# Kernel tuning notes

Measured on AMD Instinct MI355X. Metric: run time of the kernel, lower is better.

The kernel has to match this reference:

```python
import jax, jax.numpy as jnp
import numpy as np

B, N, D, H = 8192, 9, 1024, 4096
# query_type '3p': num_layer=3, edges (h_ind, r_ind, t_ind), no negation, simple_graph=False
EDGES = [(2, 3, 4), (4, 5, 6), (6, 7, 8)]
NUM_LAYER = 3
EPS = 0.1


def setup_inputs() -> dict:
    key = jax.random.key(0)
    k1, k2, k3 = jax.random.split(key, 3)
    scale1 = 1.0 / np.sqrt(D)
    scale2 = 1.0 / np.sqrt(H)
    return {
        "node_embedding": jax.random.normal(k1, (B, N, D), dtype=jnp.float32),
        "W1": jax.random.normal(k2, (D, H), dtype=jnp.float32) * scale1,
        "b1": jnp.zeros((H,), dtype=jnp.float32),
        "W2": jax.random.normal(k3, (H, D), dtype=jnp.float32) * scale2,
        "b2": jnp.zeros((D,), dtype=jnp.float32),
    }


def reference(node_embedding, W1, b1, W2, b2):
    # message passing: for each edge, tail gets estimate_tail(h, r) = h + r,
    # head gets estimate_head(t, r) = t - r (mp_lhs=True, mp_rel=False).
    # The num_layer loop re-appends identical messages, so sum = NUM_LAYER * per-edge sum.
    msgs = {}
    for h, r, t in EDGES:
        he = node_embedding[:, h]   # [B, D]
        re_ = node_embedding[:, r]
        te = node_embedding[:, t]
        msgs.setdefault(t, []).append(he + re_)   # estimate_tail_emb
        msgs.setdefault(h, []).append(te - re_)   # estimate_head_emb

    def mlp(x):
        return jax.nn.relu(x @ W1 + b1) @ W2 + b2

    terms = sorted(msgs.keys())  # [2, 4, 6, 8] for '3p'
    outs = []
    for t in terms:
        agg = NUM_LAYER * sum(msgs[t]) + node_embedding[:, t] * EPS  # agg_func='sum'
        outs.append(mlp(agg))
    return jnp.stack(outs, axis=0)  # [num_terms, B, D]
```

## Files before the change

kernel.cpp:

```cpp
#include <hip/hip_runtime.h>
#include <hip/hip_bf16.h>

typedef __hip_bfloat16 bf16;
typedef __attribute__((ext_vector_type(8))) short short8;
typedef __attribute__((ext_vector_type(4))) short short4v;
typedef __attribute__((ext_vector_type(4))) float floatx4;

#define BQ 8192
#define ND 9
#define DD 1024
#define HH 4096
#define MM 32768

__device__ __forceinline__ short f2bf(float f) {
  unsigned u = __float_as_uint(f);
  u = (u + 0x7fff + ((u >> 16) & 1)) >> 16;
  return (short)u;
}

__device__ __forceinline__ void async16(const void* g, void* l) {
  __builtin_amdgcn_global_load_lds(
      (const __attribute__((address_space(1))) void*)g,
      (__attribute__((address_space(3))) void*)l, 16, 0, 0);
}

__global__ __launch_bounds__(256) void build_x(const float* __restrict__ emb,
                                               bf16* __restrict__ X) {
  int b = blockIdx.x;
  int d = threadIdx.x * 4;
  const float* base = emb + (size_t)b * (ND * DD) + d;

  float e[7][4];
#pragma unroll
  for (int k = 0; k < 7; ++k) *(float4*)e[k] = *(const float4*)(base + (k + 2) * DD);

  auto store = [&](int t, const float* v) {
    short4v o;
#pragma unroll
    for (int c = 0; c < 4; ++c) o[c] = f2bf(v[c]);
    *(short4v*)(X + ((size_t)t * BQ + b) * DD + d) = o;
  };

  float o0[4], o1[4], o2[4], o3[4];
#pragma unroll
  for (int c = 0; c < 4; ++c) {
    o0[c] = 0.1f * e[0][c] - 3.f * e[1][c] + 3.f * e[2][c];
    o1[c] = 3.f * e[0][c] + 3.f * e[1][c] + 0.1f * e[2][c] - 3.f * e[3][c] + 3.f * e[4][c];
    o2[c] = 3.f * e[2][c] + 3.f * e[3][c] + 0.1f * e[4][c] - 3.f * e[5][c] + 3.f * e[6][c];
    o3[c] = 3.f * e[4][c] + 3.f * e[5][c] + 0.1f * e[6][c];
  }
  store(0, o0); store(1, o1); store(2, o2); store(3, o3);
}

__global__ void transpose_f2b(const float* __restrict__ src, bf16* __restrict__ dst,
                              int rows, int cols) {
  __shared__ float t[32][33];
  int c0 = blockIdx.x * 32, r0 = blockIdx.y * 32;
  int tx = threadIdx.x, ty = threadIdx.y;
  t[ty][tx] = src[(size_t)(r0 + ty) * cols + (c0 + tx)];
  __syncthreads();
  short v = f2bf(t[tx][ty]);
  dst[(size_t)(c0 + ty) * rows + (r0 + tx)] = *(bf16*)&v;
}

template <int RELU, typename OutT, int K, int N, int LOGNX>
__global__ __launch_bounds__(512, 2) void gemm256(const bf16* __restrict__ A,
                                                  const bf16* __restrict__ Bt,
                                                  const float* __restrict__ bias,
                                                  OutT* __restrict__ C) {
  constexpr int NT = K / 64;
  __shared__ bf16 sm[65536];
  char* smc = (char*)sm;
  const bf16* smb = (const bf16*)sm;

  const int tid = threadIdx.x;
  const int l = tid & 63;
  const int wv = tid >> 6;

  const int G = gridDim.x;
  const int bid = blockIdx.x;
  const int gb = (bid & 7) * (G >> 3) + (bid >> 3);
  const int n0 = (gb & ((1 << LOGNX) - 1)) * 256;
  const int m0 = (gb >> LOGNX) * 256;

  const int rowb = wv * 8 + (l >> 3);
  const int kx = ((l & 7) ^ ((l >> 3) & 7)) << 3;
  const bf16* pA = A + (size_t)(m0 + rowb) * K + kx;
  const bf16* pB = Bt + (size_t)(n0 + rowb) * K + kx;
  const int wlo = wv * 1024;

  const int ra = ((wv >> 1) * 32 + (l & 15)) * 64;
  const int rb = ((wv & 1) * 64 + (l & 15)) * 64;
  const int kg = l >> 4;
  const int sx = l & 7;

  floatx4 acc[4][8];
#pragma unroll
  for (int q = 0; q < 4; ++q)
#pragma unroll
    for (int f = 0; f < 8; ++f)
#pragma unroll
      for (int r = 0; r < 4; ++r) acc[q][f][r] = 0.f;

#define STG(GP, LO)                                            \
  do {                                                         \
    async16((GP), smc + (LO) + wlo);                           \
    async16((GP) + (size_t)64 * K, smc + (LO) + wlo + 8192);   \
  } while (0)

#define RD_A(dst, REG, BUFE)                                                   \
  _Pragma("unroll") for (int mf = 0; mf < 2; ++mf)                             \
  _Pragma("unroll") for (int ks = 0; ks < 2; ++ks)                             \
      dst[mf][ks] = *(const short8*)(smb + (BUFE) + (REG) + ra + mf * 1024 +   \
                                     ((((ks << 2) + kg) ^ sx) << 3));

#define RD_B(dst, REG, BUFE)                                                   \
  _Pragma("unroll") for (int nf = 0; nf < 4; ++nf)                             \
  _Pragma("unroll") for (int ks = 0; ks < 2; ++ks)                             \
      dst[nf][ks] = *(const short8*)(smb + (BUFE) + (REG) + rb + nf * 1024 +   \
                                     ((((ks << 2) + kg) ^ sx) << 3));

#define MF(AF, BF, Q)                                                          \
  __builtin_amdgcn_s_setprio(1);                                               \
  _Pragma("unroll") for (int ks = 0; ks < 2; ++ks)                             \
  _Pragma("unroll") for (int mf = 0; mf < 2; ++mf)                             \
  _Pragma("unroll") for (int nf = 0; nf < 4; ++nf)                             \
      acc[Q][mf * 4 + nf] = __builtin_amdgcn_mfma_f32_16x16x32_bf16(           \
          AF[mf][ks], BF[nf][ks], acc[Q][mf * 4 + nf], 0, 0, 0);               \
  __builtin_amdgcn_s_setprio(0);

#define TILE(tt, EC, BN)                                                       \
  do {                                                                         \
    short8 a0[2][2], a1[2][2], b0[4][2], b1[4][2];                             \
    RD_A(a0, 0, EC);                                                           \
    RD_B(b0, 16384, EC);                                                       \
    RD_A(a1, 8192, EC);                                                        \
    RD_B(b1, 24576, EC);                                                       \
    if ((tt) + 1 < NT) {                                                       \
      const size_t ko = (size_t)((tt) + 1) * 64;                               \
      STG(pA + ko, BN);                                                        \
      STG(pA + (size_t)128 * K + ko, (BN) + 16384);                            \
      STG(pB + ko, (BN) + 32768);                                              \
      STG(pB + (size_t)128 * K + ko, (BN) + 49152);                            \
    }                                                                          \
    MF(a0, b0, 0);                                                             \
    MF(a1, b0, 1);                                                             \
    MF(a1, b1, 2);                                                             \
    MF(a0, b1, 3);                                                             \
    __syncthreads();                                                           \
  } while (0)

  STG(pA, 0);
  STG(pA + (size_t)128 * K, 16384);
  STG(pB, 32768);
  STG(pB + (size_t)128 * K, 49152);
  __syncthreads();

#pragma unroll 1
  for (int t = 0; t < NT; t += 2) {
    TILE(t, 0, 65536);
    TILE(t + 1, 32768, 0);
  }

  const int col0 = n0 + (wv & 1) * 64 + (l & 15);
  const int row0 = m0 + (wv >> 1) * 32 + ((l >> 4) << 2);
#pragma unroll
  for (int q = 0; q < 4; ++q) {
    const int qa = (q == 1 || q == 2) ? 1 : 0;
    const int qb = (q >= 2) ? 1 : 0;
#pragma unroll
    for (int nf = 0; nf < 4; ++nf) {
      const int col = col0 + qb * 128 + nf * 16;
      const float bv = bias[col];
#pragma unroll
      for (int mf = 0; mf < 2; ++mf) {
#pragma unroll
        for (int r = 0; r < 4; ++r) {
          const int row = row0 + qa * 128 + mf * 16 + r;
          float v = acc[q][mf * 4 + nf][r] + bv;
          if (RELU) v = fmaxf(v, 0.f);
          if constexpr (sizeof(OutT) == 2) {
            short s = f2bf(v);
            C[(size_t)row * N + col] = *(OutT*)&s;
          } else {
            C[(size_t)row * N + col] = *(OutT*)&v;
          }
        }
      }
    }
  }
#undef STG
#undef RD_A
#undef RD_B
#undef MF
#undef TILE
}

extern "C" void kernel_launch(void* const* d_in, const int* in_sizes, int n_in,
                              void* d_out, int out_size, void* d_ws, size_t ws_size,
                              hipStream_t stream) {
  const float* emb = (const float*)d_in[0];
  const float* W1  = (const float*)d_in[1];
  const float* b1  = (const float*)d_in[2];
  const float* W2  = (const float*)d_in[3];
  const float* b2  = (const float*)d_in[4];
  float* out = (float*)d_out;

  char* ws = (char*)d_ws;
  bf16* X   = (bf16*)(ws);
  bf16* Y   = (bf16*)(ws + (size_t)67108864);
  bf16* W1t = (bf16*)(ws + (size_t)67108864 + (size_t)268435456);
  bf16* W2t = (bf16*)(ws + (size_t)67108864 + (size_t)268435456 + (size_t)8388608);

  build_x<<<dim3(BQ), dim3(256), 0, stream>>>(emb, X);
  transpose_f2b<<<dim3(HH / 32, DD / 32), dim3(32, 32), 0, stream>>>(W1, W1t, DD, HH);
  transpose_f2b<<<dim3(DD / 32, HH / 32), dim3(32, 32), 0, stream>>>(W2, W2t, HH, DD);
  gemm256<1, bf16, DD, HH, 4><<<dim3((MM / 256) * (HH / 256)), dim3(512), 0, stream>>>(X, W1t, b1, Y);
  gemm256<0, float, HH, DD, 2><<<dim3((MM / 256) * (DD / 256)), dim3(512), 0, stream>>>(Y, W2t, b2, out);
}
```

Measured before the change: 1.141 ms.

## Restructure GEMM main loop into phased ping-pong schedule with finer-grained prefetch

Replaces the two-tile unrolled loop, which issued all next-tile loads and then ran a full syncthreads, with a per-iteration four-phase schedule. Each phase reads one quarter of the LDS fragments, issues one sub-tile global-to-LDS load (some two tiles ahead), then runs an MFMA block between explicit s_barriers and sched_barriers. Manual vmcnt waits let loads stay in flight across iterations. The aim is better overlap of global loads, LDS reads and MFMA work, at the cost of more barriers per tile and fragile buffer-reuse ordering.

After: 938.0 us. 1.22x faster.

```diff
diff --git a/kernel.cpp b/kernel.cpp
--- a/kernel.cpp
+++ b/kernel.cpp
@@ -108,17 +108,15 @@
     async16((GP) + (size_t)64 * K, smc + (LO) + wlo + 8192);   \
   } while (0)
 
-#define RD_A(dst, REG, BUFE)                                                   \
+#define RD_A2(dst, REG, BUFE, KS)                                              \
   _Pragma("unroll") for (int mf = 0; mf < 2; ++mf)                             \
-  _Pragma("unroll") for (int ks = 0; ks < 2; ++ks)                             \
-      dst[mf][ks] = *(const short8*)(smb + (BUFE) + (REG) + ra + mf * 1024 +   \
-                                     ((((ks << 2) + kg) ^ sx) << 3));
-
-#define RD_B(dst, REG, BUFE)                                                   \
+      dst[mf][KS] = *(const short8*)(smb + (BUFE) + (REG) + ra + mf * 1024 +   \
+                                     (((((KS) << 2) + kg) ^ sx) << 3));
+
+#define RD_B2(dst, REG, BUFE, KS)                                              \
   _Pragma("unroll") for (int nf = 0; nf < 4; ++nf)                             \
-  _Pragma("unroll") for (int ks = 0; ks < 2; ++ks)                             \
-      dst[nf][ks] = *(const short8*)(smb + (BUFE) + (REG) + rb + nf * 1024 +   \
-                                     ((((ks << 2) + kg) ^ sx) << 3));
+      dst[nf][KS] = *(const short8*)(smb + (BUFE) + (REG) + rb + nf * 1024 +   \
+                                     (((((KS) << 2) + kg) ^ sx) << 3));
 
 #define MF(AF, BF, Q)                                                          \
   __builtin_amdgcn_s_setprio(1);                                               \
@@ -129,37 +127,61 @@
           AF[mf][ks], BF[nf][ks], acc[Q][mf * 4 + nf], 0, 0, 0);               \
   __builtin_amdgcn_s_setprio(0);
 
-#define TILE(tt, EC, BN)                                                       \
-  do {                                                                         \
-    short8 a0[2][2], a1[2][2], b0[4][2], b1[4][2];                             \
-    RD_A(a0, 0, EC);                                                           \
-    RD_B(b0, 16384, EC);                                                       \
-    RD_A(a1, 8192, EC);                                                        \
-    RD_B(b1, 24576, EC);                                                       \
-    if ((tt) + 1 < NT) {                                                       \
-      const size_t ko = (size_t)((tt) + 1) * 64;                               \
-      STG(pA + ko, BN);                                                        \
-      STG(pA + (size_t)128 * K + ko, (BN) + 16384);                            \
-      STG(pB + ko, (BN) + 32768);                                              \
-      STG(pB + (size_t)128 * K + ko, (BN) + 49152);                            \
-    }                                                                          \
-    MF(a0, b0, 0);                                                             \
-    MF(a1, b0, 1);                                                             \
-    MF(a1, b1, 2);                                                             \
-    MF(a0, b1, 3);                                                             \
-    __syncthreads();                                                           \
-  } while (0)
-
+#define BAR() __builtin_amdgcn_s_barrier()
+#define SBAR0() __builtin_amdgcn_sched_barrier(0)
+#define VM4() asm volatile("s_waitcnt vmcnt(4)" ::: "memory")
+#define VM0() asm volatile("s_waitcnt vmcnt(0)" ::: "memory")
+
+  STG(pB, 32768);
+  STG(pA + (size_t)128 * K, 16384);
   STG(pA, 0);
-  STG(pA + (size_t)128 * K, 16384);
-  STG(pB, 32768);
   STG(pB + (size_t)128 * K, 49152);
-  __syncthreads();
+  STG(pB + 64, 65536 + 32768);
+  STG(pA + (size_t)128 * K + 64, 65536 + 16384);
+  VM4();
+  BAR();
 
 #pragma unroll 1
-  for (int t = 0; t < NT; t += 2) {
-    TILE(t, 0, 65536);
-    TILE(t + 1, 32768, 0);
+  for (int t = 0; t < NT; ++t) {
+    const int be = (t & 1) << 15;
+    const int bnB = ((t + 1) & 1) << 16;
+    const int bcB = (t & 1) << 16;
+    short8 a0[2][2], a1[2][2], b0[4][2], b1[4][2];
+
+    SBAR0();
+    RD_A2(a0, 0, be, 0); RD_B2(b0, 16384, be, 0);
+    RD_A2(a0, 0, be, 1); RD_B2(b0, 16384, be, 1);
+    if (t + 1 < NT) STG(pA + (size_t)(t + 1) * 64, bnB);
+    BAR();
+    MF(a0, b0, 0);
+    SBAR0();
+    BAR();
+
+    SBAR0();
+    RD_A2(a1, 8192, be, 0);
+    RD_A2(a1, 8192, be, 1);
+    if (t + 1 < NT) STG(pB + (size_t)128 * K + (size_t)(t + 1) * 64, bnB + 49152);
+    BAR();
+    MF(a1, b0, 1);
+    SBAR0();
+    BAR();
+
+    SBAR0();
+    RD_B2(b1, 24576, be, 0);
+    RD_B2(b1, 24576, be, 1);
+    if (t + 2 < NT) STG(pB + (size_t)(t + 2) * 64, bcB + 32768);
+    BAR();
+    MF(a1, b1, 2);
+    SBAR0();
+    BAR();
+
+    SBAR0();
+    if (t + 2 < NT) STG(pA + (size_t)128 * K + (size_t)(t + 2) * 64, bcB + 16384);
+    BAR();
+    MF(a0, b1, 3);
+    SBAR0();
+    if (t + 2 < NT) { VM4(); } else { VM0(); }
+    BAR();
   }
 
   const int col0 = n0 + (wv & 1) * 64 + (l & 15);
@@ -190,10 +212,13 @@
     }
   }
 #undef STG
-#undef RD_A
-#undef RD_B
+#undef RD_A2
+#undef RD_B2
 #undef MF
-#undef TILE
+#undef BAR
+#undef SBAR0
+#undef VM4
+#undef VM0
 }
 
 extern "C" void kernel_launch(void* const* d_in, const int* in_sizes, int n_in,
```
